# Optimization experiments

Measured on AMD Instinct MI355X. Metric: run time of the kernel, lower is better.

Reference implementation:

```python
import jax, jax.numpy as jnp
import numpy as np
from jax import lax


def _conv(x, w, pad):
    # NCHW / OIHW conv, stride 1
    return lax.conv_general_dilated(
        x, w, window_strides=(1, 1), padding=((pad, pad), (pad, pad)),
        dimension_numbers=("NCHW", "OIHW", "NCHW"))


def setup_inputs() -> dict:
    key = jax.random.key(0)
    k1, k2, k3, k4 = jax.random.split(key, 4)
    B, C, H, W = 16, 64, 128, 128
    OUT = 64
    x = jax.random.normal(k1, (B, C, H, W), jnp.float32)
    w_off = jax.random.normal(k2, (2 * C, C, 3, 3), jnp.float32) * 0.01  # offset conv, init std 0.01
    w_conv = jax.random.normal(k3, (OUT, C, 3, 3), jnp.float32) * 0.05
    b_conv = jax.random.normal(k4, (OUT,), jnp.float32) * 0.01
    return {"x": x, "w_off": w_off, "w_conv": w_conv, "b_conv": b_conv}


def _deform(x, w_off):
    B, C, H, W = x.shape
    off = _conv(x, w_off, 1)                      # (B, 2C, H, W)
    # Faithful to torch .view(-1, H, W, 2): raw row-major memory reinterpretation
    off = off.reshape(B * C, H * W, 2)            # (BC, HW, 2) -> (row_off, col_off)
    gr, gc = jnp.meshgrid(jnp.arange(H), jnp.arange(W), indexing="ij")
    grid = jnp.stack([gr.reshape(-1), gc.reshape(-1)], -1).astype(x.dtype)  # (HW, 2)
    coords = off + grid                           # (BC, HW, 2)
    rows = jnp.clip(coords[..., 0], 0, H - 1)
    cols = jnp.clip(coords[..., 1], 0, W - 1)
    r0 = jnp.floor(rows); r1 = jnp.ceil(rows)
    c0 = jnp.floor(cols); c1 = jnp.ceil(cols)
    xf = x.reshape(B * C, H * W)

    def gather(r, c):
        idx = lax.stop_gradient((r * W + c).astype(jnp.int32))
        return jnp.take_along_axis(xf, idx, axis=1)

    v_lt = gather(r0, c0)   # (floor row, floor col)
    v_rb = gather(r1, c1)   # (ceil row,  ceil col)
    v_lb = gather(r0, c1)   # (floor row, ceil col)
    v_rt = gather(r1, c0)   # (ceil row,  floor col)
    fr = rows - r0
    fc = cols - c0
    vals_t = fr * (v_rt - v_lt) + v_lt
    vals_b = fr * (v_rb - v_lb) + v_lb
    mapped = fc * (vals_b - vals_t) + vals_t      # (BC, HW)
    return mapped.reshape(B, C, H, W)


def reference(x, w_off, w_conv, b_conv):
    xd = _deform(x, w_off)
    return _conv(xd, w_conv, 1) + b_conv[None, :, None, None]
```

## Files before the change

kernel.cpp:

```cpp
#include <hip/hip_runtime.h>

typedef _Float16 f16;
typedef _Float16 half8 __attribute__((ext_vector_type(8)));
typedef _Float16 f16x2 __attribute__((ext_vector_type(2)));
typedef float f32x4 __attribute__((ext_vector_type(4)));
typedef int i32x4 __attribute__((ext_vector_type(4)));
typedef unsigned short ushort_t;


__global__ __launch_bounds__(256) void pack_w_k(
    const float* __restrict__ w_off, const float* __restrict__ w_conv,
    f16* __restrict__ W1p, f16* __restrict__ W2p)
{
    int t = blockIdx.x * 256 + threadIdx.x;
    if (t < 73728) {
        int tap = t >> 13, oc = (t >> 6) & 127, ic = t & 63;
        W1p[t] = (f16)w_off[(oc * 64 + ic) * 9 + tap];
    } else {
        int t2 = t - 73728;
        int tap = t2 >> 12, oc = (t2 >> 6) & 63, ic = t2 & 63;
        W2p[t2] = (f16)w_conv[(oc * 64 + ic) * 9 + tap];
    }
}

__global__ __launch_bounds__(256) void transpose_k(
    const float* __restrict__ x, f16* __restrict__ xT)
{
    __shared__ float lds[64 * 132];
    const int b = blockIdx.x >> 7, h = blockIdx.x & 127;
    const int tid = threadIdx.x;
    const float4* x4 = (const float4*)x;
    for (int i = tid; i < 2048; i += 256) {
        int ic = i >> 5, wq = i & 31;
        float4 v = x4[(b * 64 + ic) * 4096 + h * 32 + wq];
        *(float4*)&lds[ic * 132 + wq * 4] = v;
    }
    __syncthreads();
    for (int i = tid; i < 1024; i += 256) {
        int w = i & 127, kg = i >> 7;
        half8 hv;
        #pragma unroll
        for (int j = 0; j < 8; ++j) hv[j] = (f16)lds[(kg * 8 + j) * 132 + w];
        *(half8*)&xT[(((size_t)(b * 128 + h) * 128 + w) << 6) + kg * 8] = hv;
    }
}

__device__ __forceinline__ float bilin(const float* __restrict__ xp, float rr, float cc) {
    rr = fminf(fmaxf(rr, 0.f), 127.f);
    cc = fminf(fmaxf(cc, 0.f), 127.f);
    const float r0f = floorf(rr), c0f = floorf(cc);
    const float r1f = ceilf(rr),  c1f = ceilf(cc);
    const int r0 = (int)r0f, r1 = (int)r1f, c0 = (int)c0f, c1 = (int)c1f;
    const float v_lt = xp[(r0 << 7) + c0];
    const float v_rt = xp[(r1 << 7) + c0];
    const float v_lb = xp[(r0 << 7) + c1];
    const float v_rb = xp[(r1 << 7) + c1];
    const float fr = rr - r0f, fc = cc - c0f;
    const float vt = fr * (v_rt - v_lt) + v_lt;
    const float vb = fr * (v_rb - v_lb) + v_lb;
    return fc * (vb - vt) + vt;
}

__global__ __launch_bounds__(256, 3) void conv1_deform_k(
    const f16* __restrict__ xT, const float* __restrict__ x,
    const f16* __restrict__ Wp, f16* __restrict__ mapped)
{
    __shared__ char lds[49920];
    ushort_t* cres = (ushort_t*)lds;

    const int tid = threadIdx.x;
    const int sr = blockIdx.x;
    const int b = blockIdx.y;
    const int t = sr >> 1, u = sr & 1;

    {
        const i32x4* s4 = (const i32x4*)xT;
        for (int s = tid; s < 3120; s += 256) {
            int kg = s & 7, q = s >> 3;
            int c = q % 130, r = q / 130;
            int rowg = sr + r - 1, wg = c - 1;
            i32x4 v = {0, 0, 0, 0};
            if ((unsigned)rowg < 128u && (unsigned)wg < 128u)
                v = s4[((b * 128 + rowg) * 128 + wg) * 8 + kg];
            int off = (q << 7) + (kg << 4);
            off ^= (c & 7) << 4;
            *(i32x4*)(lds + off) = v;
        }
    }
    __syncthreads();

    const int lane = tid & 63, wv = tid >> 6;
    const int l15 = lane & 15, l4 = lane >> 4;
    const int ocb = wv * 32 + l15;

    f32x4 acc[2][8];
    #pragma unroll
    for (int m = 0; m < 2; ++m)
        #pragma unroll
        for (int n = 0; n < 8; ++n) acc[m][n] = {0.f, 0.f, 0.f, 0.f};

    half8 a_cur[2], a_nxt[2];
    #pragma unroll
    for (int m = 0; m < 2; ++m)
        a_cur[m] = *(const half8*)&Wp[(0 * 128 + ocb + m * 16) * 64 + l4 * 8];

    #pragma unroll
    for (int step = 0; step < 18; ++step) {
        const int tap = step >> 1, ks = step & 1;
        const int ky = tap / 3, kx = tap % 3;
        if (step < 17) {
            const int tap1 = (step + 1) >> 1, ks1 = (step + 1) & 1;
            #pragma unroll
            for (int m = 0; m < 2; ++m)
                a_nxt[m] = *(const half8*)&Wp[(tap1 * 128 + ocb + m * 16) * 64 + ks1 * 32 + l4 * 8];
        }
        #pragma unroll
        for (int n = 0; n < 8; ++n) {
            const int c = n * 16 + l15 + kx;
            int off = ((ky * 130 + c) << 7) + (ks << 6) + (l4 << 4);
            off ^= (c & 7) << 4;
            const half8 bf = *(const half8*)(lds + off);
            acc[0][n] = __builtin_amdgcn_mfma_f32_16x16x32_f16(a_cur[0], bf, acc[0][n], 0, 0, 0);
            acc[1][n] = __builtin_amdgcn_mfma_f32_16x16x32_f16(a_cur[1], bf, acc[1][n], 0, 0, 0);
        }
        #pragma unroll
        for (int m = 0; m < 2; ++m) a_cur[m] = a_nxt[m];
    }

    __syncthreads();

    #pragma unroll
    for (int m = 0; m < 2; ++m) {
        const int oc0 = wv * 32 + m * 16 + l4 * 4;
        #pragma unroll
        for (int n = 0; n < 8; ++n) {
            const int pix = n * 16 + l15;
            const int base = pix * 130 + oc0;
            f16x2 p0; p0[0] = (f16)acc[m][n][0]; p0[1] = (f16)acc[m][n][1];
            f16x2 p1; p1[0] = (f16)acc[m][n][2]; p1[1] = (f16)acc[m][n][3];
            *(f16x2*)&cres[base]     = p0;
            *(f16x2*)&cres[base + 2] = p1;
        }
    }
    __syncthreads();

    {
        const int hsel = tid >> 7;
        const int c0 = ((tid >> 6) & 1) * 32;
        const int w_off = tid & 63;
        const int w_out = u * 64 + w_off;
        const int h_out = t + hsel * 64;
        const int wq = 2 * w_off;
        const float hb = (float)h_out, wb = (float)w_out;
        f16* mp = mapped + ((((size_t)b << 14) + h_out * 128 + w_out) << 6) + c0;

        #pragma unroll
        for (int j = 0; j < 4; ++j) {
            half8 ov;
            #pragma unroll
            for (int e = 0; e < 8; ++e) {
                const int c = c0 + j * 8 + e;
                const float R  = (float)*(const f16*)&cres[wq * 130 + 2 * c + hsel];
                const float Cf = (float)*(const f16*)&cres[(wq + 1) * 130 + 2 * c + hsel];
                const float* xp = x + (((size_t)b * 64 + c) << 14);
                ov[e] = (f16)bilin(xp, R + hb, Cf + wb);
            }
            *(half8*)&mp[j * 8] = ov;
        }
    }
}

__global__ __launch_bounds__(256, 3) void conv2_k(
    const f16* __restrict__ src, const f16* __restrict__ Wp,
    const float* __restrict__ bias, float* __restrict__ out)
{
    __shared__ char lds[49920];
    const int tid = threadIdx.x;
    const int h = blockIdx.x;
    const int b = blockIdx.y;

    {
        const i32x4* s4 = (const i32x4*)src;
        for (int s = tid; s < 3120; s += 256) {
            int kg = s & 7, q = s >> 3;
            int c = q % 130, r = q / 130;
            int rowg = h + r - 1, wg = c - 1;
            i32x4 v = {0, 0, 0, 0};
            if ((unsigned)rowg < 128u && (unsigned)wg < 128u)
                v = s4[((b * 128 + rowg) * 128 + wg) * 8 + kg];
            int off = (q << 7) + (kg << 4);
            off ^= (c & 7) << 4;
            *(i32x4*)(lds + off) = v;
        }
    }
    __syncthreads();

    const int lane = tid & 63, wv = tid >> 6;
    const int l15 = lane & 15, l4 = lane >> 4;
    const int wm = wv >> 1, wn = wv & 1;
    const int ocb = wm * 32 + l15;
    const int pixb = wn * 64;

    f32x4 acc[2][4];
    #pragma unroll
    for (int m = 0; m < 2; ++m)
        #pragma unroll
        for (int n = 0; n < 4; ++n) acc[m][n] = {0.f, 0.f, 0.f, 0.f};

    half8 a_cur[2], a_nxt[2];
    #pragma unroll
    for (int m = 0; m < 2; ++m)
        a_cur[m] = *(const half8*)&Wp[(0 * 64 + ocb + m * 16) * 64 + l4 * 8];

    #pragma unroll
    for (int step = 0; step < 18; ++step) {
        const int tap = step >> 1, ks = step & 1;
        const int ky = tap / 3, kx = tap % 3;
        if (step < 17) {
            const int tap1 = (step + 1) >> 1, ks1 = (step + 1) & 1;
            #pragma unroll
            for (int m = 0; m < 2; ++m)
                a_nxt[m] = *(const half8*)&Wp[(tap1 * 64 + ocb + m * 16) * 64 + ks1 * 32 + l4 * 8];
        }
        #pragma unroll
        for (int n = 0; n < 4; ++n) {
            const int c = pixb + n * 16 + l15 + kx;
            int off = ((ky * 130 + c) << 7) + (ks << 6) + (l4 << 4);
            off ^= (c & 7) << 4;
            const half8 bf = *(const half8*)(lds + off);
            acc[0][n] = __builtin_amdgcn_mfma_f32_16x16x32_f16(a_cur[0], bf, acc[0][n], 0, 0, 0);
            acc[1][n] = __builtin_amdgcn_mfma_f32_16x16x32_f16(a_cur[1], bf, acc[1][n], 0, 0, 0);
        }
        #pragma unroll
        for (int m = 0; m < 2; ++m) a_cur[m] = a_nxt[m];
    }

    #pragma unroll
    for (int m = 0; m < 2; ++m) {
        #pragma unroll
        for (int i = 0; i < 4; ++i) {
            const int oc = wm * 32 + m * 16 + l4 * 4 + i;
            const float bb = bias[oc];
            #pragma unroll
            for (int n = 0; n < 4; ++n) {
                const int pix = pixb + n * 16 + l15;
                out[(((size_t)b * 64 + oc) << 14) + h * 128 + pix] = acc[m][n][i] + bb;
            }
        }
    }
}

extern "C" void kernel_launch(void* const* d_in, const int* in_sizes, int n_in,
                              void* d_out, int out_size, void* d_ws, size_t ws_size,
                              hipStream_t stream) {
    const float* x      = (const float*)d_in[0];
    const float* w_off  = (const float*)d_in[1];
    const float* w_conv = (const float*)d_in[2];
    const float* b_conv = (const float*)d_in[3];
    float* out = (float*)d_out;

    char* ws = (char*)d_ws;
    f16* xT     = (f16*)ws;
    f16* mapped = (f16*)(ws + 33554432);
    f16* W1p    = (f16*)(ws + 67108864);
    f16* W2p    = (f16*)(ws + 67108864 + 147456);

    pack_w_k<<<432, 256, 0, stream>>>(w_off, w_conv, W1p, W2p);
    transpose_k<<<2048, 256, 0, stream>>>(x, xT);
    conv1_deform_k<<<dim3(128, 16), 256, 0, stream>>>(xT, x, W1p, mapped);
    conv2_k<<<dim3(128, 16), 256, 0, stream>>>(mapped, W2p, b_conv, out);
}
```

Measured before the change: 271.6 us.

## Split conv tiles into half-row blocks and fuse weight packing into transpose

Both conv kernels now process half a row (64 columns) per block instead of a full row. This halves the LDS footprint and accumulator registers, doubles the grid, and raises the occupancy hints to 4 and 6 blocks. The weight-packing kernel is merged into the transpose kernel as extra blocks, saving one launch. The cost is more halo reloading per output pixel and the deform gather being spread over smaller tiles.

```diff
diff --git a/kernel.cpp b/kernel.cpp
--- a/kernel.cpp
+++ b/kernel.cpp
@@ -8,27 +8,27 @@
 typedef unsigned short ushort_t;
 
 
-__global__ __launch_bounds__(256) void pack_w_k(
+__global__ __launch_bounds__(256) void transpose_pack_k(
+    const float* __restrict__ x, f16* __restrict__ xT,
     const float* __restrict__ w_off, const float* __restrict__ w_conv,
     f16* __restrict__ W1p, f16* __restrict__ W2p)
 {
-    int t = blockIdx.x * 256 + threadIdx.x;
-    if (t < 73728) {
-        int tap = t >> 13, oc = (t >> 6) & 127, ic = t & 63;
-        W1p[t] = (f16)w_off[(oc * 64 + ic) * 9 + tap];
-    } else {
-        int t2 = t - 73728;
-        int tap = t2 >> 12, oc = (t2 >> 6) & 63, ic = t2 & 63;
-        W2p[t2] = (f16)w_conv[(oc * 64 + ic) * 9 + tap];
-    }
-}
-
-__global__ __launch_bounds__(256) void transpose_k(
-    const float* __restrict__ x, f16* __restrict__ xT)
-{
     __shared__ float lds[64 * 132];
+    const int tid = threadIdx.x;
+    if (blockIdx.x >= 2048) {
+        for (int t = (blockIdx.x - 2048) * 256 + tid; t < 110592; t += 16384) {
+            if (t < 73728) {
+                int tap = t >> 13, oc = (t >> 6) & 127, ic = t & 63;
+                W1p[t] = (f16)w_off[(oc * 64 + ic) * 9 + tap];
+            } else {
+                int t2 = t - 73728;
+                int tap = t2 >> 12, oc = (t2 >> 6) & 63, ic = t2 & 63;
+                W2p[t2] = (f16)w_conv[(oc * 64 + ic) * 9 + tap];
+            }
+        }
+        return;
+    }
     const int b = blockIdx.x >> 7, h = blockIdx.x & 127;
-    const int tid = threadIdx.x;
     const float4* x4 = (const float4*)x;
     for (int i = tid; i < 2048; i += 256) {
         int ic = i >> 5, wq = i & 31;
@@ -61,24 +61,25 @@
     return fc * (vb - vt) + vt;
 }
 
-__global__ __launch_bounds__(256, 3) void conv1_deform_k(
+__global__ __launch_bounds__(256, 4) void conv1_deform_k(
     const f16* __restrict__ xT, const float* __restrict__ x,
     const f16* __restrict__ Wp, f16* __restrict__ mapped)
 {
-    __shared__ char lds[49920];
+    __shared__ char lds[25344];
     ushort_t* cres = (ushort_t*)lds;
 
     const int tid = threadIdx.x;
-    const int sr = blockIdx.x;
+    const int sr = blockIdx.x >> 1, ph = blockIdx.x & 1;
     const int b = blockIdx.y;
     const int t = sr >> 1, u = sr & 1;
+    const int col0 = ph * 64;
 
     {
         const i32x4* s4 = (const i32x4*)xT;
-        for (int s = tid; s < 3120; s += 256) {
+        for (int s = tid; s < 1584; s += 256) {
             int kg = s & 7, q = s >> 3;
-            int c = q % 130, r = q / 130;
-            int rowg = sr + r - 1, wg = c - 1;
+            int c = q % 66, r = q / 66;
+            int rowg = sr + r - 1, wg = col0 + c - 1;
             i32x4 v = {0, 0, 0, 0};
             if ((unsigned)rowg < 128u && (unsigned)wg < 128u)
                 v = s4[((b * 128 + rowg) * 128 + wg) * 8 + kg];
@@ -93,11 +94,11 @@
     const int l15 = lane & 15, l4 = lane >> 4;
     const int ocb = wv * 32 + l15;
 
-    f32x4 acc[2][8];
-    #pragma unroll
-    for (int m = 0; m < 2; ++m)
-        #pragma unroll
-        for (int n = 0; n < 8; ++n) acc[m][n] = {0.f, 0.f, 0.f, 0.f};
+    f32x4 acc[2][4];
+    #pragma unroll
+    for (int m = 0; m < 2; ++m)
+        #pragma unroll
+        for (int n = 0; n < 4; ++n) acc[m][n] = {0.f, 0.f, 0.f, 0.f};
 
     half8 a_cur[2], a_nxt[2];
     #pragma unroll
@@ -115,9 +116,9 @@
                 a_nxt[m] = *(const half8*)&Wp[(tap1 * 128 + ocb + m * 16) * 64 + ks1 * 32 + l4 * 8];
         }
         #pragma unroll
-        for (int n = 0; n < 8; ++n) {
+        for (int n = 0; n < 4; ++n) {
             const int c = n * 16 + l15 + kx;
-            int off = ((ky * 130 + c) << 7) + (ks << 6) + (l4 << 4);
+            int off = ((ky * 66 + c) << 7) + (ks << 6) + (l4 << 4);
             off ^= (c & 7) << 4;
             const half8 bf = *(const half8*)(lds + off);
             acc[0][n] = __builtin_amdgcn_mfma_f32_16x16x32_f16(a_cur[0], bf, acc[0][n], 0, 0, 0);
@@ -133,7 +134,7 @@
     for (int m = 0; m < 2; ++m) {
         const int oc0 = wv * 32 + m * 16 + l4 * 4;
         #pragma unroll
-        for (int n = 0; n < 8; ++n) {
+        for (int n = 0; n < 4; ++n) {
             const int pix = n * 16 + l15;
             const int base = pix * 130 + oc0;
             f16x2 p0; p0[0] = (f16)acc[m][n][0]; p0[1] = (f16)acc[m][n][1];
@@ -145,23 +146,23 @@
     __syncthreads();
 
     {
-        const int hsel = tid >> 7;
-        const int c0 = ((tid >> 6) & 1) * 32;
-        const int w_off = tid & 63;
-        const int w_out = u * 64 + w_off;
+        const int w_rel = tid & 31;
+        const int hsel = (tid >> 5) & 1;
+        const int cg = tid >> 6;
+        const int w_out = u * 64 + 32 * ph + w_rel;
         const int h_out = t + hsel * 64;
-        const int wq = 2 * w_off;
+        const int q = 2 * w_rel;
         const float hb = (float)h_out, wb = (float)w_out;
-        f16* mp = mapped + ((((size_t)b << 14) + h_out * 128 + w_out) << 6) + c0;
-
-        #pragma unroll
-        for (int j = 0; j < 4; ++j) {
+        f16* mp = mapped + ((((size_t)b << 14) + h_out * 128 + w_out) << 6) + cg * 16;
+
+        #pragma unroll
+        for (int j = 0; j < 2; ++j) {
             half8 ov;
             #pragma unroll
             for (int e = 0; e < 8; ++e) {
-                const int c = c0 + j * 8 + e;
-                const float R  = (float)*(const f16*)&cres[wq * 130 + 2 * c + hsel];
-                const float Cf = (float)*(const f16*)&cres[(wq + 1) * 130 + 2 * c + hsel];
+                const int c = cg * 16 + j * 8 + e;
+                const float R  = (float)*(const f16*)&cres[q * 130 + 2 * c + hsel];
+                const float Cf = (float)*(const f16*)&cres[(q + 1) * 130 + 2 * c + hsel];
                 const float* xp = x + (((size_t)b * 64 + c) << 14);
                 ov[e] = (f16)bilin(xp, R + hb, Cf + wb);
             }
@@ -170,21 +171,22 @@
     }
 }
 
-__global__ __launch_bounds__(256, 3) void conv2_k(
+__global__ __launch_bounds__(256, 6) void conv2_k(
     const f16* __restrict__ src, const f16* __restrict__ Wp,
     const float* __restrict__ bias, float* __restrict__ out)
 {
-    __shared__ char lds[49920];
+    __shared__ char lds[25344];
     const int tid = threadIdx.x;
-    const int h = blockIdx.x;
+    const int h = blockIdx.x >> 1, ph = blockIdx.x & 1;
     const int b = blockIdx.y;
+    const int col0 = ph * 64;
 
     {
         const i32x4* s4 = (const i32x4*)src;
-        for (int s = tid; s < 3120; s += 256) {
+        for (int s = tid; s < 1584; s += 256) {
             int kg = s & 7, q = s >> 3;
-            int c = q % 130, r = q / 130;
-            int rowg = h + r - 1, wg = c - 1;
+            int c = q % 66, r = q / 66;
+            int rowg = h + r - 1, wg = col0 + c - 1;
             i32x4 v = {0, 0, 0, 0};
             if ((unsigned)rowg < 128u && (unsigned)wg < 128u)
                 v = s4[((b * 128 + rowg) * 128 + wg) * 8 + kg];
@@ -199,13 +201,13 @@
     const int l15 = lane & 15, l4 = lane >> 4;
     const int wm = wv >> 1, wn = wv & 1;
     const int ocb = wm * 32 + l15;
-    const int pixb = wn * 64;
-
-    f32x4 acc[2][4];
-    #pragma unroll
-    for (int m = 0; m < 2; ++m)
-        #pragma unroll
-        for (int n = 0; n < 4; ++n) acc[m][n] = {0.f, 0.f, 0.f, 0.f};
+    const int pixb = wn * 32;
+
+    f32x4 acc[2][2];
+    #pragma unroll
+    for (int m = 0; m < 2; ++m)
+        #pragma unroll
+        for (int n = 0; n < 2; ++n) acc[m][n] = {0.f, 0.f, 0.f, 0.f};
 
     half8 a_cur[2], a_nxt[2];
     #pragma unroll
@@ -223,9 +225,9 @@
                 a_nxt[m] = *(const half8*)&Wp[(tap1 * 64 + ocb + m * 16) * 64 + ks1 * 32 + l4 * 8];
         }
         #pragma unroll
-        for (int n = 0; n < 4; ++n) {
+        for (int n = 0; n < 2; ++n) {
             const int c = pixb + n * 16 + l15 + kx;
-            int off = ((ky * 130 + c) << 7) + (ks << 6) + (l4 << 4);
+            int off = ((ky * 66 + c) << 7) + (ks << 6) + (l4 << 4);
             off ^= (c & 7) << 4;
             const half8 bf = *(const half8*)(lds + off);
             acc[0][n] = __builtin_amdgcn_mfma_f32_16x16x32_f16(a_cur[0], bf, acc[0][n], 0, 0, 0);
@@ -242,8 +244,8 @@
             const int oc = wm * 32 + m * 16 + l4 * 4 + i;
             const float bb = bias[oc];
             #pragma unroll
-            for (int n = 0; n < 4; ++n) {
-                const int pix = pixb + n * 16 + l15;
+            for (int n = 0; n < 2; ++n) {
+                const int pix = col0 + pixb + n * 16 + l15;
                 out[(((size_t)b * 64 + oc) << 14) + h * 128 + pix] = acc[m][n][i] + bb;
             }
         }
@@ -265,8 +267,7 @@
     f16* W1p    = (f16*)(ws + 67108864);
     f16* W2p    = (f16*)(ws + 67108864 + 147456);
 
-    pack_w_k<<<432, 256, 0, stream>>>(w_off, w_conv, W1p, W2p);
-    transpose_k<<<2048, 256, 0, stream>>>(x, xT);
-    conv1_deform_k<<<dim3(128, 16), 256, 0, stream>>>(xT, x, W1p, mapped);
-    conv2_k<<<dim3(128, 16), 256, 0, stream>>>(mapped, W2p, b_conv, out);
-}
+    transpose_pack_k<<<2112, 256, 0, stream>>>(x, xT, w_off, w_conv, W1p, W2p);
+    conv1_deform_k<<<dim3(256, 16), 256, 0, stream>>>(xT, x, W1p, mapped);
+    conv2_k<<<dim3(256, 16), 256, 0, stream>>>(mapped, W2p, b_conv, out);
+}
```

Measured after the change: 315.5 us. 16.2% more time.
